# Optimization experiments

Hardware: AMD Instinct MI355X
Metric: run time of the kernel (lower is better)

The kernel has to match this reference:

```python
import jax, jax.numpy as jnp
import numpy as np

H, K, D, M = 16, 64, 1024, 4096
S, B = 2048, 4
EPS = 1e-5


def _ln(x, g, b):
    mu = jnp.mean(x, axis=-1, keepdims=True)
    var = jnp.var(x, axis=-1, keepdims=True)
    return (x - mu) / jnp.sqrt(var + EPS) * g + b


def setup_inputs() -> dict:
    key = jax.random.key(0)
    ks = jax.random.split(key, 8)
    std = 0.02
    x = jax.random.normal(ks[0], (S, B, D), jnp.float32)
    mask = jnp.zeros((S, S), jnp.float32)  # additive attention mask, broadcasts over (H*B, S, S)
    wq = jax.random.normal(ks[1], (H * K, D), jnp.float32) * std
    wk = jax.random.normal(ks[2], (H * K, D), jnp.float32) * std
    wv = jax.random.normal(ks[3], (H * K, D), jnp.float32) * std
    wc = jax.random.normal(ks[4], (D, H * K), jnp.float32) * std
    w1_w = jax.random.normal(ks[5], (M, D), jnp.float32) * std
    w1_b = jnp.zeros((M,), jnp.float32)
    w2_w = jax.random.normal(ks[6], (D, M), jnp.float32) * std
    w2_b = jnp.zeros((D,), jnp.float32)
    ln1_g = jnp.ones((D,), jnp.float32)
    ln1_b = jnp.zeros((D,), jnp.float32)
    ln2_g = jnp.ones((D,), jnp.float32)
    ln2_b = jnp.zeros((D,), jnp.float32)
    return dict(x=x, mask=mask, wq=wq, wk=wk, wv=wv, wc=wc, w1_w=w1_w, w1_b=w1_b,
                w2_w=w2_w, w2_b=w2_b, ln1_g=ln1_g, ln1_b=ln1_b, ln2_g=ln2_g, ln2_b=ln2_b)


def reference(x, mask, wq, wk, wv, wc, w1_w, w1_b, w2_w, w2_b, ln1_g, ln1_b, ln2_g, ln2_b):
    s, b, _ = x.shape
    q = (x @ wq.T).reshape(s, b, H, K)
    k = (x @ wk.T).reshape(s, b, H, K)
    v = (x @ wv.T).reshape(s, b, H, K)
    # scores: (B, H, S, S); mask (S, S) broadcasts over batch and heads as in torch
    scores = jnp.einsum('sbhk,tbhk->bhst', q, k) / jnp.sqrt(jnp.float32(K)) + mask
    alpha = jax.nn.softmax(scores, axis=-1)
    av = jnp.einsum('bhst,tbhk->sbhk', alpha, v).reshape(s, b, H * K)
    u = _ln(av @ wc.T + x, ln1_g, ln1_b)
    z = jax.nn.relu(u @ w1_w.T + w1_b) @ w2_w.T + w2_b
    return _ln(z + u, ln2_g, ln2_b)
```

## Files before the change

### kernel.cpp

```cpp
#include <hip/hip_runtime.h>
#include <math.h>

#define H_  16
#define K_  64
#define D_  1024
#define M_  4096
#define S_  2048
#define B_  4
#define N_  8192
#define HK_ 1024

typedef __attribute__((ext_vector_type(8))) short bfrag;
typedef __attribute__((ext_vector_type(4))) float f4;

typedef __attribute__((address_space(1))) const void g_void;
typedef __attribute__((address_space(3))) void s_void;

__device__ __forceinline__ float bf2f(unsigned short u){
  union { unsigned int i; float f; } x; x.i = ((unsigned int)u) << 16; return x.f;
}
__device__ __forceinline__ unsigned short f2bf(float f){
  unsigned int u = __float_as_uint(f);
  return (unsigned short)((u + 0x7fffu + ((u >> 16) & 1u)) >> 16);
}
__device__ __forceinline__ unsigned int pack2(float a, float b){
  return (unsigned int)f2bf(a) | ((unsigned int)f2bf(b) << 16);
}
__device__ __forceinline__ void gload16(const void* g, void* l){
  __builtin_amdgcn_global_load_lds((g_void*)g, (s_void*)l, 16, 0, 0);
}

__global__ __launch_bounds__(256) void castk(const float* __restrict__ in,
                                             unsigned short* __restrict__ out){
  int i = (blockIdx.x * 256 + threadIdx.x) * 4;
  float4 v = *(const float4*)(in + i);
  *(uint2*)(out + i) = make_uint2(pack2(v.x, v.y), pack2(v.z, v.w));
}

__global__ __launch_bounds__(256) void mscale(const float* __restrict__ in,
                                              float* __restrict__ out){
  int i = (blockIdx.x * 256 + threadIdx.x) * 4;
  float4 v = *(const float4*)(in + i);
  const float c = 1.44269504f;
  v.x *= c; v.y *= c; v.z *= c; v.w *= c;
  *(float4*)(out + i) = v;
}

template<int EPI>
__global__ __launch_bounds__(256) void mgemm(
    const unsigned short* __restrict__ A, const unsigned short* __restrict__ W,
    const float* __restrict__ bias, const void* __restrict__ res,
    unsigned short* __restrict__ C, int Kdim, int Ncols)
{
  __shared__ unsigned short sA[4096];
  __shared__ unsigned short sB[4096];
  const int tid  = threadIdx.x;
  const int wave = tid >> 6, ln = tid & 63;
  const int lr   = ln & 15, quad = ln >> 4;
  const int m0   = blockIdx.y * 128, n0 = blockIdx.x * 128;
  const int wr   = (wave >> 1) * 64, wc = (wave & 1) * 64;
  const int segr = ln >> 2, segc = (ln & 3) * 8;
  const int sg   = wave * 2;

  const unsigned short* A0 = A + (size_t)(m0 + sg*16      + segr) * Kdim + segc;
  const unsigned short* A1 = A + (size_t)(m0 + sg*16 + 16 + segr) * Kdim + segc;
  const unsigned short* W0 = W + (size_t)(n0 + sg*16      + segr) * Kdim + segc;
  const unsigned short* W1 = W + (size_t)(n0 + sg*16 + 16 + segr) * Kdim + segc;

  const f4 zero = {0.f, 0.f, 0.f, 0.f};
  f4 acc[4][4];
  #pragma unroll
  for (int i=0;i<4;i++)
    #pragma unroll
    for (int j=0;j<4;j++) acc[i][j] = zero;

  for (int k0 = 0; k0 < Kdim; k0 += 32){
    gload16(A0 + k0, &sA[sg*512]);
    gload16(A1 + k0, &sA[sg*512 + 512]);
    gload16(W0 + k0, &sB[sg*512]);
    gload16(W1 + k0, &sB[sg*512 + 512]);
    __syncthreads();
    bfrag af[4], bf[4];
    #pragma unroll
    for (int i=0;i<4;i++) af[i] = *(const bfrag*)&sA[(wr + i*16 + lr)*32 + quad*8];
    #pragma unroll
    for (int j=0;j<4;j++) bf[j] = *(const bfrag*)&sB[(wc + j*16 + lr)*32 + quad*8];
    #pragma unroll
    for (int i=0;i<4;i++)
      #pragma unroll
      for (int j=0;j<4;j++)
        acc[i][j] = __builtin_amdgcn_mfma_f32_16x16x32_bf16(af[i], bf[j], acc[i][j], 0, 0, 0);
    __syncthreads();
  }

  #pragma unroll
  for (int i=0;i<4;i++){
    #pragma unroll
    for (int j=0;j<4;j++){
      #pragma unroll
      for (int r=0;r<4;r++){
        const int m = m0 + wr + i*16 + quad*4 + r;
        const int n = n0 + wc + j*16 + lr;
        float t = acc[i][j][r];
        if (EPI == 0){
          const int s = m >> 2, b = m & 3, h = n >> 6, kk = n & 63;
          C[(((size_t)(b*16 + h)) * S_ + s) * 64 + kk] = f2bf(t);
        } else {
          const size_t off = (size_t)m * Ncols + n;
          if (EPI == 1) t += ((const float*)res)[off];
          if (EPI == 2) t = fmaxf(t + bias[n], 0.f);
          if (EPI == 3) t += bias[n] + bf2f(((const unsigned short*)res)[off]);
          C[off] = f2bf(t);
        }
      }
    }
  }
}

__global__ __launch_bounds__(256) void vtrans(const unsigned short* __restrict__ v,
                                              unsigned short* __restrict__ vT){
  const int tid = threadIdx.x;
  const int wave = tid >> 6, ln = tid & 63;
  const int bh = blockIdx.y;
  const int s  = blockIdx.x * 64 + ln;
  const int d0 = wave * 16;
  unsigned short tmp[16];
  const unsigned short* src = v + ((size_t)bh * S_ + s) * 64 + d0;
  *(uint4*)&tmp[0] = ((const uint4*)src)[0];
  *(uint4*)&tmp[8] = ((const uint4*)src)[1];
  unsigned short* dst = vT + (size_t)bh * 64 * S_ + s;
  #pragma unroll
  for (int e = 0; e < 16; e++)
    dst[(size_t)(d0 + e) * S_] = tmp[e];
}

__global__ __launch_bounds__(256) void fattn(
    const unsigned short* __restrict__ qg, const unsigned short* __restrict__ kg,
    const unsigned short* __restrict__ vT, const float* __restrict__ mb,
    unsigned short* __restrict__ av)
{
  __shared__ unsigned short Ks[2][4096];
  __shared__ unsigned short VTs[2][4096];
  __shared__ unsigned short Ps[4*32*72];
  const int tid  = threadIdx.x;
  const int wave = tid >> 6, ln = tid & 63;
  const int lr   = ln & 15, quad = ln >> 4;
  const int bh   = blockIdx.y;
  const int b    = bh >> 4, h = bh & 15;
  const int s0   = blockIdx.x * 128;
  const size_t base  = (size_t)bh * S_ * 64;
  const size_t tbase = (size_t)bh * 64 * S_;
  const int qw = s0 + wave*32;

  bfrag aq[2][2];
  #pragma unroll
  for (int qb=0;qb<2;qb++)
    #pragma unroll
    for (int hh=0;hh<2;hh++)
      aq[qb][hh] = *(const bfrag*)(qg + base + (size_t)(qw + qb*16 + lr)*64 + hh*32 + quad*8);

  const f4 zero = {0.f, 0.f, 0.f, 0.f};
  f4 acc[2][4];
  #pragma unroll
  for (int qb=0;qb<2;qb++)
    #pragma unroll
    for (int nb=0;nb<4;nb++) acc[qb][nb] = zero;
  float lsum[2][4];
  #pragma unroll
  for (int qb=0;qb<2;qb++)
    #pragma unroll
    for (int r=0;r<4;r++) lsum[qb][r] = 0.f;

  const int strow = wave*16 + (ln >> 3);
  const int scz   = ((ln & 7) ^ (ln >> 3)) * 8;
  const int rxor  = lr & 7;

  unsigned short* const psw = &Ps[wave*2304];

  const float* mrow[2][4];
  #pragma unroll
  for (int qb=0;qb<2;qb++)
    #pragma unroll
    for (int r=0;r<4;r++)
      mrow[qb][r] = mb + (size_t)(qw + qb*16 + quad*4 + r) * S_ + lr;

  auto stage = [&](int bufn, int t0n){
    unsigned short* kd = &Ks[bufn][(wave*16)*64];
    unsigned short* vd = &VTs[bufn][(wave*16)*64];
    gload16(kg + base  + (size_t)(t0n + strow    )*64 + scz, kd);
    gload16(kg + base  + (size_t)(t0n + strow + 8)*64 + scz, kd + 512);
    gload16(vT + tbase + (size_t)(strow    )*S_ + t0n + scz, vd);
    gload16(vT + tbase + (size_t)(strow + 8)*S_ + t0n + scz, vd + 512);
  };

  stage(0, 0);
  int cur = 0;

  for (int t0 = 0; t0 < S_; t0 += 64){
    __syncthreads();

    float mreg[2][4][4];
    #pragma unroll
    for (int qb=0;qb<2;qb++)
      #pragma unroll
      for (int r=0;r<4;r++)
        #pragma unroll
        for (int tb=0;tb<4;tb++)
          mreg[qb][r][tb] = mrow[qb][r][t0 + tb*16];

    if (t0 + 64 < S_) stage(cur ^ 1, t0 + 64);

    const unsigned short* Kc = Ks[cur];
    const unsigned short* Vc = VTs[cur];

    bfrag kf[4][2];
    #pragma unroll
    for (int tb=0;tb<4;tb++)
      #pragma unroll
      for (int hh=0;hh<2;hh++)
        kf[tb][hh] = *(const bfrag*)&Kc[(tb*16 + lr)*64 + (((hh*4 + quad) ^ rxor))*8];

    bfrag vf[4][2];
    #pragma unroll
    for (int nb=0;nb<4;nb++)
      #pragma unroll
      for (int hh=0;hh<2;hh++)
        vf[nb][hh] = *(const bfrag*)&Vc[(nb*16 + lr)*64 + (((hh*4 + quad) ^ rxor))*8];

    #pragma unroll
    for (int qb=0;qb<2;qb++){
      f4 sc[4];
      __builtin_amdgcn_s_setprio(1);
      #pragma unroll
      for (int tb=0;tb<4;tb++){
        f4 t = zero;
        t = __builtin_amdgcn_mfma_f32_16x16x32_bf16(aq[qb][0], kf[tb][0], t, 0, 0, 0);
        t = __builtin_amdgcn_mfma_f32_16x16x32_bf16(aq[qb][1], kf[tb][1], t, 0, 0, 0);
        sc[tb] = t;
      }
      __builtin_amdgcn_s_setprio(0);
      #pragma unroll
      for (int tb=0;tb<4;tb++){
        float p0 = __builtin_amdgcn_exp2f(fmaf(sc[tb][0], 0.18033688f, mreg[qb][0][tb]));
        float p1 = __builtin_amdgcn_exp2f(fmaf(sc[tb][1], 0.18033688f, mreg[qb][1][tb]));
        float p2 = __builtin_amdgcn_exp2f(fmaf(sc[tb][2], 0.18033688f, mreg[qb][2][tb]));
        float p3 = __builtin_amdgcn_exp2f(fmaf(sc[tb][3], 0.18033688f, mreg[qb][3][tb]));
        lsum[qb][0] += p0; lsum[qb][1] += p1;
        lsum[qb][2] += p2; lsum[qb][3] += p3;
        unsigned int pkA, pkB;
        asm("v_cvt_pk_bf16_f32 %0, %1, %2" : "=v"(pkA) : "v"(p0), "v"(p1));
        asm("v_cvt_pk_bf16_f32 %0, %1, %2" : "=v"(pkB) : "v"(p2), "v"(p3));
        unsigned short* pp = &psw[(qb*16 + quad*4)*72 + tb*16 + lr];
        pp[0]   = (unsigned short)pkA;
        pp[72]  = (unsigned short)(pkA >> 16);
        pp[144] = (unsigned short)pkB;
        pp[216] = (unsigned short)(pkB >> 16);
      }
    }

    __builtin_amdgcn_s_setprio(1);
    #pragma unroll
    for (int qb=0;qb<2;qb++){
      bfrag ap0 = *(const bfrag*)&psw[(qb*16 + lr)*72 + quad*8];
      bfrag ap1 = *(const bfrag*)&psw[(qb*16 + lr)*72 + 32 + quad*8];
      #pragma unroll
      for (int nb=0;nb<4;nb++){
        acc[qb][nb] = __builtin_amdgcn_mfma_f32_16x16x32_bf16(ap0, vf[nb][0], acc[qb][nb], 0, 0, 0);
        acc[qb][nb] = __builtin_amdgcn_mfma_f32_16x16x32_bf16(ap1, vf[nb][1], acc[qb][nb], 0, 0, 0);
      }
    }
    __builtin_amdgcn_s_setprio(0);
    cur ^= 1;
  }

  #pragma unroll
  for (int qb=0;qb<2;qb++)
    #pragma unroll
    for (int r=0;r<4;r++){
      float l = lsum[qb][r];
      l += __shfl_xor(l, 1);
      l += __shfl_xor(l, 2);
      l += __shfl_xor(l, 4);
      l += __shfl_xor(l, 8);
      const float inv = 1.f / l;
      const int qrow = qw + qb*16 + quad*4 + r;
      #pragma unroll
      for (int nb=0;nb<4;nb++)
        av[((size_t)qrow * B_ + b) * HK_ + h*64 + nb*16 + lr] = f2bf(acc[qb][nb][r] * inv);
    }
}

template<int OUTF32>
__global__ __launch_bounds__(256) void lnk(
    const unsigned short* __restrict__ pre, const float* __restrict__ g,
    const float* __restrict__ be, void* __restrict__ out)
{
  __shared__ float red[256];
  const int row = blockIdx.x;
  const int tid = threadIdx.x;
  const unsigned short* p = pre + (size_t)row * D_;
  uint2 raw = *(const uint2*)(p + tid*4);
  float x[4] = { bf2f(raw.x & 0xffffu), bf2f(raw.x >> 16),
                 bf2f(raw.y & 0xffffu), bf2f(raw.y >> 16) };
  red[tid] = x[0] + x[1] + x[2] + x[3];
  __syncthreads();
  for (int q = 128; q > 0; q >>= 1){
    if (tid < q) red[tid] += red[tid + q];
    __syncthreads();
  }
  const float mu = red[0] * (1.f / (float)D_);
  __syncthreads();
  float d0 = x[0]-mu, d1 = x[1]-mu, d2 = x[2]-mu, d3 = x[3]-mu;
  red[tid] = d0*d0 + d1*d1 + d2*d2 + d3*d3;
  __syncthreads();
  for (int q = 128; q > 0; q >>= 1){
    if (tid < q) red[tid] += red[tid + q];
    __syncthreads();
  }
  const float rstd = rsqrtf(red[0] * (1.f / (float)D_) + 1e-5f);
  const int c = tid * 4;
  #pragma unroll
  for (int j=0;j<4;j++){
    float y = (x[j] - mu) * rstd * g[c + j] + be[c + j];
    if (OUTF32) ((float*)out)[(size_t)row * D_ + c + j] = y;
    else ((unsigned short*)out)[(size_t)row * D_ + c + j] = f2bf(y);
  }
}

extern "C" void kernel_launch(void* const* d_in, const int* in_sizes, int n_in,
                              void* d_out, int out_size, void* d_ws, size_t ws_size,
                              hipStream_t stream) {
  const float* x    = (const float*)d_in[0];
  const float* mask = (const float*)d_in[1];
  const float* wq   = (const float*)d_in[2];
  const float* wk   = (const float*)d_in[3];
  const float* wv   = (const float*)d_in[4];
  const float* wc   = (const float*)d_in[5];
  const float* w1w  = (const float*)d_in[6];
  const float* w1b  = (const float*)d_in[7];
  const float* w2w  = (const float*)d_in[8];
  const float* w2b  = (const float*)d_in[9];
  const float* g1   = (const float*)d_in[10];
  const float* b1   = (const float*)d_in[11];
  const float* g2   = (const float*)d_in[12];
  const float* b2   = (const float*)d_in[13];

  unsigned short* ws = (unsigned short*)d_ws;
  unsigned short* xb   = ws + 0;
  unsigned short* wqb  = ws + 8388608;
  unsigned short* wkb  = ws + 9437184;
  unsigned short* wvb  = ws + 10485760;
  unsigned short* wcb  = ws + 11534336;
  unsigned short* q    = ws + 12582912;
  unsigned short* k    = ws + 20971520;
  unsigned short* v    = ws + 29360128;
  unsigned short* w1wb = ws + 37748736;
  unsigned short* w2wb = ws + 41943040;
  unsigned short* u    = ws + 46137344;
  unsigned short* z    = ws + 54525952;
  unsigned short* vT   = z;
  unsigned short* avb  = ws + 0;
  unsigned short* t1   = ws + 12582912;
  unsigned short* h1   = ws + 0;
  float*          mb   = (float*)(ws + 46137344);

  castk<<<8192, 256, 0, stream>>>(x,   xb);
  castk<<<1024, 256, 0, stream>>>(wq,  wqb);
  castk<<<1024, 256, 0, stream>>>(wk,  wkb);
  castk<<<1024, 256, 0, stream>>>(wv,  wvb);
  castk<<<1024, 256, 0, stream>>>(wc,  wcb);
  castk<<<4096, 256, 0, stream>>>(w1w, w1wb);
  castk<<<4096, 256, 0, stream>>>(w2w, w2wb);
  mscale<<<4096, 256, 0, stream>>>(mask, mb);

  mgemm<0><<<dim3(8, 64), 256, 0, stream>>>(xb, wqb, nullptr, nullptr, q, D_, HK_);
  mgemm<0><<<dim3(8, 64), 256, 0, stream>>>(xb, wkb, nullptr, nullptr, k, D_, HK_);
  mgemm<0><<<dim3(8, 64), 256, 0, stream>>>(xb, wvb, nullptr, nullptr, v, D_, HK_);

  vtrans<<<dim3(S_/64, 64), 256, 0, stream>>>(v, vT);
  fattn<<<dim3(S_/128, B_*H_), 256, 0, stream>>>(q, k, vT, mb, avb);

  mgemm<1><<<dim3(8, 64), 256, 0, stream>>>(avb, wcb, nullptr, x, t1, HK_, D_);
  lnk<0><<<dim3(N_), 256, 0, stream>>>(t1, g1, b1, u);

  mgemm<2><<<dim3(32, 64), 256, 0, stream>>>(u, w1wb, w1b, nullptr, h1, D_, M_);

  mgemm<3><<<dim3(8, 64), 256, 0, stream>>>(h1, w2wb, w2b, u, z, M_, D_);
  lnk<1><<<dim3(N_), 256, 0, stream>>>(z, g2, b2, d_out);
}
```

Before: 650.6 us.

## Switch flash attention to 32x32x16 MFMA with register-resident P via permlane swap

Reworks the attention kernel to use 32x32x16 bf16 MFMAs and computes S^T (K as A operand, Q as B) so each lane holds one query row. The softmax probabilities are packed to bf16 and rearranged between lane halves with v_permlane32_swap, so they feed the PV MFMA straight from registers instead of going through a per-wave LDS staging buffer. Mask loads become float4 vector loads, the row sum needs only a single cross-half shuffle, and output stores are vectorized. This removes LDS round-trips and barriers-free scratch traffic but raises register pressure and relies on correct fragment layout mapping.

Result: slower. 697.5 us (+7.2%).

```diff
diff --git a/kernel.cpp b/kernel.cpp
--- a/kernel.cpp
+++ b/kernel.cpp
@@ -12,6 +12,7 @@
 
 typedef __attribute__((ext_vector_type(8))) short bfrag;
 typedef __attribute__((ext_vector_type(4))) float f4;
+typedef __attribute__((ext_vector_type(16))) float f16v;
 
 typedef __attribute__((address_space(1))) const void g_void;
 typedef __attribute__((address_space(3))) void s_void;
@@ -141,48 +142,34 @@
 {
   __shared__ unsigned short Ks[2][4096];
   __shared__ unsigned short VTs[2][4096];
-  __shared__ unsigned short Ps[4*32*72];
   const int tid  = threadIdx.x;
   const int wave = tid >> 6, ln = tid & 63;
-  const int lr   = ln & 15, quad = ln >> 4;
+  const int l31  = ln & 31, hi = ln >> 5;
   const int bh   = blockIdx.y;
   const int b    = bh >> 4, h = bh & 15;
   const int s0   = blockIdx.x * 128;
   const size_t base  = (size_t)bh * S_ * 64;
   const size_t tbase = (size_t)bh * 64 * S_;
-  const int qw = s0 + wave*32;
-
-  bfrag aq[2][2];
-  #pragma unroll
-  for (int qb=0;qb<2;qb++)
-    #pragma unroll
-    for (int hh=0;hh<2;hh++)
-      aq[qb][hh] = *(const bfrag*)(qg + base + (size_t)(qw + qb*16 + lr)*64 + hh*32 + quad*8);
-
-  const f4 zero = {0.f, 0.f, 0.f, 0.f};
-  f4 acc[2][4];
-  #pragma unroll
-  for (int qb=0;qb<2;qb++)
-    #pragma unroll
-    for (int nb=0;nb<4;nb++) acc[qb][nb] = zero;
-  float lsum[2][4];
-  #pragma unroll
-  for (int qb=0;qb<2;qb++)
-    #pragma unroll
-    for (int r=0;r<4;r++) lsum[qb][r] = 0.f;
+  const int qw   = s0 + wave*32;
+  const int qrow = qw + l31;
+
+  bfrag qf[4];
+  #pragma unroll
+  for (int kk=0;kk<4;kk++)
+    qf[kk] = *(const bfrag*)(qg + base + (size_t)qrow*64 + kk*16 + hi*8);
+
+  f16v acc[2];
+  #pragma unroll
+  for (int db=0;db<2;db++)
+    #pragma unroll
+    for (int r=0;r<16;r++) acc[db][r] = 0.f;
+  float lsum = 0.f;
 
   const int strow = wave*16 + (ln >> 3);
   const int scz   = ((ln & 7) ^ (ln >> 3)) * 8;
-  const int rxor  = lr & 7;
-
-  unsigned short* const psw = &Ps[wave*2304];
-
-  const float* mrow[2][4];
-  #pragma unroll
-  for (int qb=0;qb<2;qb++)
-    #pragma unroll
-    for (int r=0;r<4;r++)
-      mrow[qb][r] = mb + (size_t)(qw + qb*16 + quad*4 + r) * S_ + lr;
+  const int rx    = ln & 7;
+
+  const float* mrow = mb + (size_t)qrow * S_;
 
   auto stage = [&](int bufn, int t0n){
     unsigned short* kd = &Ks[bufn][(wave*16)*64];
@@ -199,94 +186,89 @@
   for (int t0 = 0; t0 < S_; t0 += 64){
     __syncthreads();
 
-    float mreg[2][4][4];
-    #pragma unroll
-    for (int qb=0;qb<2;qb++)
-      #pragma unroll
-      for (int r=0;r<4;r++)
-        #pragma unroll
-        for (int tb=0;tb<4;tb++)
-          mreg[qb][r][tb] = mrow[qb][r][t0 + tb*16];
+    float4 mk[2][4];
+    #pragma unroll
+    for (int tb=0;tb<2;tb++)
+      #pragma unroll
+      for (int g=0;g<4;g++)
+        mk[tb][g] = *(const float4*)(mrow + t0 + tb*32 + g*8 + hi*4);
 
     if (t0 + 64 < S_) stage(cur ^ 1, t0 + 64);
 
     const unsigned short* Kc = Ks[cur];
     const unsigned short* Vc = VTs[cur];
 
-    bfrag kf[4][2];
-    #pragma unroll
-    for (int tb=0;tb<4;tb++)
-      #pragma unroll
-      for (int hh=0;hh<2;hh++)
-        kf[tb][hh] = *(const bfrag*)&Kc[(tb*16 + lr)*64 + (((hh*4 + quad) ^ rxor))*8];
-
-    bfrag vf[4][2];
-    #pragma unroll
-    for (int nb=0;nb<4;nb++)
-      #pragma unroll
-      for (int hh=0;hh<2;hh++)
-        vf[nb][hh] = *(const bfrag*)&Vc[(nb*16 + lr)*64 + (((hh*4 + quad) ^ rxor))*8];
-
-    #pragma unroll
-    for (int qb=0;qb<2;qb++){
-      f4 sc[4];
+    union fragU { unsigned int u[4]; bfrag f; };
+    fragU pf[2][2];
+
+    #pragma unroll
+    for (int tb=0;tb<2;tb++){
+      bfrag kf[4];
+      #pragma unroll
+      for (int kk=0;kk<4;kk++)
+        kf[kk] = *(const bfrag*)&Kc[(tb*32 + l31)*64 + ((kk*2 + hi) ^ rx)*8];
+
+      f16v sc;
+      #pragma unroll
+      for (int r=0;r<16;r++) sc[r] = 0.f;
       __builtin_amdgcn_s_setprio(1);
       #pragma unroll
-      for (int tb=0;tb<4;tb++){
-        f4 t = zero;
-        t = __builtin_amdgcn_mfma_f32_16x16x32_bf16(aq[qb][0], kf[tb][0], t, 0, 0, 0);
-        t = __builtin_amdgcn_mfma_f32_16x16x32_bf16(aq[qb][1], kf[tb][1], t, 0, 0, 0);
-        sc[tb] = t;
+      for (int kk=0;kk<4;kk++)
+        sc = __builtin_amdgcn_mfma_f32_32x32x16_bf16(kf[kk], qf[kk], sc, 0, 0, 0);
+      __builtin_amdgcn_s_setprio(0);
+
+      float p[16];
+      #pragma unroll
+      for (int g=0;g<4;g++){
+        p[g*4+0] = __builtin_amdgcn_exp2f(fmaf(sc[g*4+0], 0.18033688f, mk[tb][g].x));
+        p[g*4+1] = __builtin_amdgcn_exp2f(fmaf(sc[g*4+1], 0.18033688f, mk[tb][g].y));
+        p[g*4+2] = __builtin_amdgcn_exp2f(fmaf(sc[g*4+2], 0.18033688f, mk[tb][g].z));
+        p[g*4+3] = __builtin_amdgcn_exp2f(fmaf(sc[g*4+3], 0.18033688f, mk[tb][g].w));
+        lsum += p[g*4+0] + p[g*4+1] + p[g*4+2] + p[g*4+3];
       }
-      __builtin_amdgcn_s_setprio(0);
-      #pragma unroll
-      for (int tb=0;tb<4;tb++){
-        float p0 = __builtin_amdgcn_exp2f(fmaf(sc[tb][0], 0.18033688f, mreg[qb][0][tb]));
-        float p1 = __builtin_amdgcn_exp2f(fmaf(sc[tb][1], 0.18033688f, mreg[qb][1][tb]));
-        float p2 = __builtin_amdgcn_exp2f(fmaf(sc[tb][2], 0.18033688f, mreg[qb][2][tb]));
-        float p3 = __builtin_amdgcn_exp2f(fmaf(sc[tb][3], 0.18033688f, mreg[qb][3][tb]));
-        lsum[qb][0] += p0; lsum[qb][1] += p1;
-        lsum[qb][2] += p2; lsum[qb][3] += p3;
-        unsigned int pkA, pkB;
-        asm("v_cvt_pk_bf16_f32 %0, %1, %2" : "=v"(pkA) : "v"(p0), "v"(p1));
-        asm("v_cvt_pk_bf16_f32 %0, %1, %2" : "=v"(pkB) : "v"(p2), "v"(p3));
-        unsigned short* pp = &psw[(qb*16 + quad*4)*72 + tb*16 + lr];
-        pp[0]   = (unsigned short)pkA;
-        pp[72]  = (unsigned short)(pkA >> 16);
-        pp[144] = (unsigned short)pkB;
-        pp[216] = (unsigned short)(pkB >> 16);
+
+      #pragma unroll
+      for (int kk2=0;kk2<2;kk2++){
+        unsigned int a0, a1, b0, b1;
+        asm("v_cvt_pk_bf16_f32 %0, %1, %2" : "=v"(a0) : "v"(p[kk2*8+0]), "v"(p[kk2*8+1]));
+        asm("v_cvt_pk_bf16_f32 %0, %1, %2" : "=v"(a1) : "v"(p[kk2*8+2]), "v"(p[kk2*8+3]));
+        asm("v_cvt_pk_bf16_f32 %0, %1, %2" : "=v"(b0) : "v"(p[kk2*8+4]), "v"(p[kk2*8+5]));
+        asm("v_cvt_pk_bf16_f32 %0, %1, %2" : "=v"(b1) : "v"(p[kk2*8+6]), "v"(p[kk2*8+7]));
+        asm("v_permlane32_swap_b32 %0, %1" : "+v"(a0), "+v"(b0));
+        asm("v_permlane32_swap_b32 %0, %1" : "+v"(a1), "+v"(b1));
+        pf[tb][kk2].u[0] = a0;
+        pf[tb][kk2].u[1] = a1;
+        pf[tb][kk2].u[2] = b0;
+        pf[tb][kk2].u[3] = b1;
       }
     }
 
     __builtin_amdgcn_s_setprio(1);
     #pragma unroll
-    for (int qb=0;qb<2;qb++){
-      bfrag ap0 = *(const bfrag*)&psw[(qb*16 + lr)*72 + quad*8];
-      bfrag ap1 = *(const bfrag*)&psw[(qb*16 + lr)*72 + 32 + quad*8];
-      #pragma unroll
-      for (int nb=0;nb<4;nb++){
-        acc[qb][nb] = __builtin_amdgcn_mfma_f32_16x16x32_bf16(ap0, vf[nb][0], acc[qb][nb], 0, 0, 0);
-        acc[qb][nb] = __builtin_amdgcn_mfma_f32_16x16x32_bf16(ap1, vf[nb][1], acc[qb][nb], 0, 0, 0);
+    for (int tb=0;tb<2;tb++)
+      #pragma unroll
+      for (int kk2=0;kk2<2;kk2++){
+        #pragma unroll
+        for (int db=0;db<2;db++){
+          bfrag vfr = *(const bfrag*)&Vc[(db*32 + l31)*64 + ((tb*4 + kk2*2 + hi) ^ rx)*8];
+          acc[db] = __builtin_amdgcn_mfma_f32_32x32x16_bf16(vfr, pf[tb][kk2].f, acc[db], 0, 0, 0);
+        }
       }
-    }
     __builtin_amdgcn_s_setprio(0);
     cur ^= 1;
   }
 
-  #pragma unroll
-  for (int qb=0;qb<2;qb++)
-    #pragma unroll
-    for (int r=0;r<4;r++){
-      float l = lsum[qb][r];
-      l += __shfl_xor(l, 1);
-      l += __shfl_xor(l, 2);
-      l += __shfl_xor(l, 4);
-      l += __shfl_xor(l, 8);
-      const float inv = 1.f / l;
-      const int qrow = qw + qb*16 + quad*4 + r;
-      #pragma unroll
-      for (int nb=0;nb<4;nb++)
-        av[((size_t)qrow * B_ + b) * HK_ + h*64 + nb*16 + lr] = f2bf(acc[qb][nb][r] * inv);
+  const float lt  = lsum + __shfl_xor(lsum, 32);
+  const float inv = 1.f / lt;
+  unsigned short* orow = av + ((size_t)qrow * B_ + b) * HK_ + h*64;
+  #pragma unroll
+  for (int db=0;db<2;db++)
+    #pragma unroll
+    for (int g=0;g<4;g++){
+      uint2 o;
+      o.x = pack2(acc[db][g*4+0]*inv, acc[db][g*4+1]*inv);
+      o.y = pack2(acc[db][g*4+2]*inv, acc[db][g*4+3]*inv);
+      *(uint2*)(orow + db*32 + g*8 + hi*4) = o;
     }
 }
 
```

## Double-buffer GEMM shared-memory tiles and fuse QKV projections into one launch

Applied to the files above, without the earlier changes.

The bf16 MFMA GEMM now keeps two LDS tile buffers per operand and prefetches the next K-slice while computing on the current one. This removes one barrier per iteration and lets global loads overlap with MFMA work. The three Q/K/V projection GEMMs become a single launch over 3072 output columns, with the epilogue sending each column range to its own head-major output. The fused launch relies on the Q/K/V weights and outputs being laid out contiguously in the workspace. Doubling the LDS tiles may also lower occupancy.

After: 598.7 us. 8.0% less time.

```diff
diff --git a/kernel.cpp b/kernel.cpp
--- a/kernel.cpp
+++ b/kernel.cpp
@@ -52,8 +52,8 @@
     const float* __restrict__ bias, const void* __restrict__ res,
     unsigned short* __restrict__ C, int Kdim, int Ncols)
 {
-  __shared__ unsigned short sA[4096];
-  __shared__ unsigned short sB[4096];
+  __shared__ unsigned short sA[2][4096];
+  __shared__ unsigned short sB[2][4096];
   const int tid  = threadIdx.x;
   const int wave = tid >> 6, ln = tid & 63;
   const int lr   = ln & 15, quad = ln >> 4;
@@ -74,23 +74,30 @@
     #pragma unroll
     for (int j=0;j<4;j++) acc[i][j] = zero;
 
+  auto stage = [&](int buf, int k0){
+    gload16(A0 + k0, &sA[buf][sg*512]);
+    gload16(A1 + k0, &sA[buf][sg*512 + 512]);
+    gload16(W0 + k0, &sB[buf][sg*512]);
+    gload16(W1 + k0, &sB[buf][sg*512 + 512]);
+  };
+
+  stage(0, 0);
+  int cur = 0;
+
   for (int k0 = 0; k0 < Kdim; k0 += 32){
-    gload16(A0 + k0, &sA[sg*512]);
-    gload16(A1 + k0, &sA[sg*512 + 512]);
-    gload16(W0 + k0, &sB[sg*512]);
-    gload16(W1 + k0, &sB[sg*512 + 512]);
     __syncthreads();
+    if (k0 + 32 < Kdim) stage(cur ^ 1, k0 + 32);
     bfrag af[4], bf[4];
     #pragma unroll
-    for (int i=0;i<4;i++) af[i] = *(const bfrag*)&sA[(wr + i*16 + lr)*32 + quad*8];
-    #pragma unroll
-    for (int j=0;j<4;j++) bf[j] = *(const bfrag*)&sB[(wc + j*16 + lr)*32 + quad*8];
+    for (int i=0;i<4;i++) af[i] = *(const bfrag*)&sA[cur][(wr + i*16 + lr)*32 + quad*8];
+    #pragma unroll
+    for (int j=0;j<4;j++) bf[j] = *(const bfrag*)&sB[cur][(wc + j*16 + lr)*32 + quad*8];
     #pragma unroll
     for (int i=0;i<4;i++)
       #pragma unroll
       for (int j=0;j<4;j++)
         acc[i][j] = __builtin_amdgcn_mfma_f32_16x16x32_bf16(af[i], bf[j], acc[i][j], 0, 0, 0);
-    __syncthreads();
+    cur ^= 1;
   }
 
   #pragma unroll
@@ -103,8 +110,9 @@
         const int n = n0 + wc + j*16 + lr;
         float t = acc[i][j][r];
         if (EPI == 0){
-          const int s = m >> 2, b = m & 3, h = n >> 6, kk = n & 63;
-          C[(((size_t)(b*16 + h)) * S_ + s) * 64 + kk] = f2bf(t);
+          const int proj = n >> 10;
+          const int s = m >> 2, b = m & 3, h = (n >> 6) & 15, kk = n & 63;
+          C[(size_t)proj*8388608 + (((size_t)(b*16 + h)) * S_ + s) * 64 + kk] = f2bf(t);
         } else {
           const size_t off = (size_t)m * Ncols + n;
           if (EPI == 1) t += ((const float*)res)[off];
@@ -373,9 +381,7 @@
   castk<<<4096, 256, 0, stream>>>(w2w, w2wb);
   mscale<<<4096, 256, 0, stream>>>(mask, mb);
 
-  mgemm<0><<<dim3(8, 64), 256, 0, stream>>>(xb, wqb, nullptr, nullptr, q, D_, HK_);
-  mgemm<0><<<dim3(8, 64), 256, 0, stream>>>(xb, wkb, nullptr, nullptr, k, D_, HK_);
-  mgemm<0><<<dim3(8, 64), 256, 0, stream>>>(xb, wvb, nullptr, nullptr, v, D_, HK_);
+  mgemm<0><<<dim3(24, 64), 256, 0, stream>>>(xb, wqb, nullptr, nullptr, q, D_, 3072);
 
   vtrans<<<dim3(S_/64, 64), 256, 0, stream>>>(v, vT);
   fattn<<<dim3(S_/128, B_*H_), 256, 0, stream>>>(q, k, vT, mb, avb);
```
